# Optimization experiments

Hardware: AMD Instinct MI355X
Metric: run time of the kernel (lower is better)

## Reference

```python
import jax, jax.numpy as jnp
import numpy as np

HIDDEN = 4096
NH = 32        # query heads
HD = 128       # head dim
NKV = 8        # kv heads
RD = 64        # rotary dim (partial rotary)
THETA = 10000.0
SEQ = 2048


def _rope(x, positions):
    # x: [S, H, HD]; neox-style rope on first RD dims of each head
    half = RD // 2
    inv_freq = 1.0 / (THETA ** (jnp.arange(half, dtype=jnp.float32) / half))
    freqs = positions.astype(jnp.float32)[:, None] * inv_freq[None, :]  # [S, half]
    cos = jnp.cos(freqs)[:, None, :]  # [S,1,half]
    sin = jnp.sin(freqs)[:, None, :]
    x_rot, x_pass = x[..., :RD], x[..., RD:]
    x1, x2 = x_rot[..., :half], x_rot[..., half:]
    o1 = x1 * cos - x2 * sin
    o2 = x2 * cos + x1 * sin
    return jnp.concatenate([o1, o2, x_pass], axis=-1)


def setup_inputs() -> dict:
    key = jax.random.key(0)
    k1, k2, k3 = jax.random.split(key, 3)
    hidden_states = jax.random.normal(k1, (SEQ, HIDDEN), dtype=jnp.float32)
    Wqkv = jax.random.normal(k2, (HIDDEN, (NH + 2 * NKV) * HD), dtype=jnp.float32) * 0.02
    Wo = jax.random.normal(k3, (NH * HD, HIDDEN), dtype=jnp.float32) * 0.02
    positions = jnp.arange(SEQ, dtype=jnp.int64)
    return {"hidden_states": hidden_states, "Wqkv": Wqkv, "Wo": Wo, "positions": positions}


def reference(hidden_states, Wqkv, Wo, positions):
    S = hidden_states.shape[0]
    qkv = hidden_states @ Wqkv  # [S, (NH+2*NKV)*HD]
    q, k, v = jnp.split(qkv, [NH * HD, NH * HD + NKV * HD], axis=-1)
    q = q.reshape(S, NH, HD)
    k = k.reshape(S, NKV, HD)
    v = v.reshape(S, NKV, HD)
    q = _rope(q, positions)
    k = _rope(k, positions)
    # GQA: expand kv heads to query heads
    g = NH // NKV
    k = jnp.repeat(k, g, axis=1)  # [S, NH, HD]
    v = jnp.repeat(v, g, axis=1)
    scale = HD ** -0.5
    scores = jnp.einsum('shd,thd->hst', q, k) * scale  # [NH, S, S]
    causal = jnp.tril(jnp.ones((S, S), dtype=bool))
    scores = jnp.where(causal[None, :, :], scores, jnp.finfo(scores.dtype).min)
    probs = jax.nn.softmax(scores, axis=-1)
    attn = jnp.einsum('hst,thd->shd', probs, v).reshape(S, NH * HD)
    return attn @ Wo
```

## Files before the change

kernel.cpp:

```cpp
#include <hip/hip_runtime.h>

#define S_LEN 2048
#define HID 4096
#define NH 32
#define NKV 8
#define HD 128
#define QKVN 6144
#define KOFF 4096
#define VOFF 5120

typedef unsigned short ushort_t;
typedef unsigned int uint_t;
typedef __attribute__((ext_vector_type(8))) short short8;
typedef __attribute__((ext_vector_type(4))) short short4v;
typedef __attribute__((ext_vector_type(4))) float float4_t;

__device__ __forceinline__ float bf2f(ushort_t u) {
    return __uint_as_float(((uint_t)u) << 16);
}
__device__ __forceinline__ uint_t f2bf(float f) {
    uint_t u = __float_as_uint(f);
    u += 0x7fffu + ((u >> 16) & 1u);
    return u >> 16;
}

__device__ __forceinline__ void gload_lds16(const ushort_t* g, ushort_t* l) {
    __builtin_amdgcn_global_load_lds(
        (const __attribute__((address_space(1))) void*)g,
        (__attribute__((address_space(3))) void*)l, 16, 0, 0);
}

__global__ void f32_to_bf16(const float4* __restrict__ in,
                            short4v* __restrict__ out) {
    int i = blockIdx.x * 256 + threadIdx.x;
    float4 v = in[i];
    short4v o;
    o[0] = (short)f2bf(v.x);
    o[1] = (short)f2bf(v.y);
    o[2] = (short)f2bf(v.z);
    o[3] = (short)f2bf(v.w);
    out[i] = o;
}

__global__ void transpose_f32_bf16(const float* __restrict__ in,
                                   ushort_t* __restrict__ out, int R, int C) {
    __shared__ float t[32][33];
    int c0 = blockIdx.x * 32, r0 = blockIdx.y * 32;
    int ci = threadIdx.x & 31, rb = threadIdx.x >> 5;
#pragma unroll
    for (int p = 0; p < 4; p++) {
        int ri = rb + p * 8;
        t[ri][ci] = in[(size_t)(r0 + ri) * C + c0 + ci];
    }
    __syncthreads();
    int cp = (threadIdx.x & 15) * 2;
    int rw = threadIdx.x >> 4;
#pragma unroll
    for (int p = 0; p < 2; p++) {
        int ri = rw + p * 16;
        uint_t w = f2bf(t[cp][ri]) | (f2bf(t[cp + 1][ri]) << 16);
        *(uint_t*)(&out[(size_t)(c0 + ri) * R + r0 + cp]) = w;
    }
}

__global__ __launch_bounds__(256, 2)
void gemm_bf16(const ushort_t* __restrict__ A, const ushort_t* __restrict__ BT,
               float* __restrict__ Cout, int M, int N, int K) {
    __shared__ __attribute__((aligned(16))) ushort_t As[128 * 32];
    __shared__ __attribute__((aligned(16))) ushort_t Bs[128 * 32];
    const int tid  = threadIdx.x;
    const int wave = tid >> 6;
    const int lane = tid & 63;
    const int quad = lane >> 4;
    const int l16  = lane & 15;
    const int m0 = blockIdx.y * 128;
    const int n0 = blockIdx.x * 128;
    const int wm = (wave & 1) * 64;
    const int wn = (wave >> 1) * 64;

    const int r0 = tid >> 2;
    const int kc = (tid & 3) * 8;
    const ushort_t* gA0 = A  + (size_t)(m0 + r0)      * K + kc;
    const ushort_t* gA1 = A  + (size_t)(m0 + r0 + 64) * K + kc;
    const ushort_t* gB0 = BT + (size_t)(n0 + r0)      * K + kc;
    const ushort_t* gB1 = BT + (size_t)(n0 + r0 + 64) * K + kc;
    ushort_t* lA0 = &As[r0 * 32 + kc];
    ushort_t* lA1 = lA0 + 64 * 32;
    ushort_t* lB0 = &Bs[r0 * 32 + kc];
    ushort_t* lB1 = lB0 + 64 * 32;

    float4_t acc[4][4] = {};

    for (int k0 = 0; k0 < K; k0 += 32) {
        gload_lds16(gA0 + k0, lA0);
        gload_lds16(gA1 + k0, lA1);
        gload_lds16(gB0 + k0, lB0);
        gload_lds16(gB1 + k0, lB1);
        __syncthreads();

        short8 af[4], bfr[4];
#pragma unroll
        for (int i = 0; i < 4; i++)
            af[i] = *(const short8*)(&As[(wm + i * 16 + l16) * 32 + quad * 8]);
#pragma unroll
        for (int j = 0; j < 4; j++)
            bfr[j] = *(const short8*)(&Bs[(wn + j * 16 + l16) * 32 + quad * 8]);
#pragma unroll
        for (int i = 0; i < 4; i++)
#pragma unroll
            for (int j = 0; j < 4; j++)
                acc[i][j] = __builtin_amdgcn_mfma_f32_16x16x32_bf16(
                    af[i], bfr[j], acc[i][j], 0, 0, 0);
        __syncthreads();
    }

#pragma unroll
    for (int i = 0; i < 4; i++)
#pragma unroll
        for (int j = 0; j < 4; j++)
#pragma unroll
            for (int r = 0; r < 4; r++) {
                int row = m0 + wm + i * 16 + quad * 4 + r;
                int col = n0 + wn + j * 16 + l16;
                Cout[(size_t)row * N + col] = acc[i][j][r];
            }
}

__global__ void rope_tab_k(float2* __restrict__ tab) {
    int idx = blockIdx.x * 256 + threadIdx.x;
    int i = idx & 31;
    int s = idx >> 5;
    float invf = exp2f(-(float)i * (13.287712379549449f / 32.0f));
    float fr = (float)s * invf;
    float c, sn;
    sincosf(fr, &sn, &c);
    tab[idx] = make_float2(c, sn);
}

#define QSC 0.12753102543918255f
__global__ void prep_q(const float* __restrict__ qkv, const float2* __restrict__ tab,
                       ushort_t* __restrict__ Qb) {
    int idx = blockIdx.x * 256 + threadIdx.x;
    int d = idx & 127;
    int s = (idx >> 7) & 2047;
    int h = idx >> 18;
    const float* row = qkv + (size_t)s * QKVN + h * HD;
    float v;
    if (d < 64) {
        int i = d & 31;
        float2 cs = tab[(s << 5) + i];
        float x1 = row[i], x2 = row[i + 32];
        v = (d < 32) ? (x1 * cs.x - x2 * cs.y) : (x2 * cs.x + x1 * cs.y);
    } else {
        v = row[d];
    }
    Qb[idx] = (ushort_t)f2bf(v * QSC);
}

__global__ void prep_k(const float* __restrict__ qkv, const float2* __restrict__ tab,
                       ushort_t* __restrict__ Kb) {
    int idx = blockIdx.x * 256 + threadIdx.x;
    int d = idx & 127;
    int t = (idx >> 7) & 2047;
    int hk = idx >> 18;
    const float* row = qkv + (size_t)t * QKVN + KOFF + hk * HD;
    float v;
    if (d < 64) {
        int i = d & 31;
        float2 cs = tab[(t << 5) + i];
        float x1 = row[i], x2 = row[i + 32];
        v = (d < 32) ? (x1 * cs.x - x2 * cs.y) : (x2 * cs.x + x1 * cs.y);
    } else {
        v = row[d];
    }
    Kb[idx] = (ushort_t)f2bf(v);
}

__global__ void prep_v(const float* __restrict__ qkv, ushort_t* __restrict__ Vt) {
    __shared__ float tile[32][33];
    int hk = blockIdx.z;
    int t0 = blockIdx.x * 32, d0 = blockIdx.y * 32;
    int ci = threadIdx.x & 31, rb = threadIdx.x >> 5;
#pragma unroll
    for (int p = 0; p < 4; p++) {
        int tr = rb + p * 8;
        tile[tr][ci] = qkv[(size_t)(t0 + tr) * QKVN + VOFF + hk * HD + d0 + ci];
    }
    __syncthreads();
#pragma unroll
    for (int p = 0; p < 4; p++) {
        int dr = rb + p * 8;
        Vt[((size_t)hk * HD + d0 + dr) * S_LEN + t0 + ci] = (ushort_t)f2bf(tile[ci][dr]);
    }
}

__global__ __launch_bounds__(256, 3)
void flash_attn(const ushort_t* __restrict__ Qb, const ushort_t* __restrict__ Kb,
                const ushort_t* __restrict__ Vt, ushort_t* __restrict__ attn) {
    __shared__ __attribute__((aligned(16))) ushort_t Ks[2][32 * 128];
    __shared__ __attribute__((aligned(16))) ushort_t Vs[2][128 * 32];

    const int h    = blockIdx.y;
    const int hk   = h >> 2;
    const int tid  = threadIdx.x;
    const int wave = tid >> 6;
    const int lane = tid & 63;
    const int quad = lane >> 4;
    const int l16  = lane & 15;
    const int bx   = (int)blockIdx.x;
    const int u    = bx + 16 * wave;
    const int qwE  = u * 32;
    const int qwO  = qwE + 16;

    const ushort_t* Qh = Qb + (size_t)h  * S_LEN * HD;
    const ushort_t* Kh = Kb + (size_t)hk * S_LEN * HD;
    const ushort_t* Vh = Vt + (size_t)hk * HD * S_LEN;

    const int krow = tid >> 4;
    const int ksrc = ((tid & 15) ^ (krow & 7)) << 3;
    const ushort_t* gK0 = Kh + (size_t)krow * HD + ksrc;
    const ushort_t* gK1 = Kh + (size_t)(krow + 16) * HD + ksrc;
    const int vrow = tid >> 2;
    const int vtb  = (tid & 3) << 3;
    const ushort_t* gV0 = Vh + (size_t)vrow * S_LEN + vtb;
    const ushort_t* gV1 = Vh + (size_t)(vrow + 64) * S_LEN + vtb;

    ushort_t* lK = &Ks[0][tid * 8];
    ushort_t* lV = &Vs[0][tid * 8];

#define STAGE(buf, t0)                                                        \
    do {                                                                      \
        gload_lds16(gK0 + (size_t)(t0) * HD, lK + (buf) * (32 * 128));        \
        gload_lds16(gK1 + (size_t)(t0) * HD, lK + (buf) * (32 * 128) + 2048); \
        gload_lds16(gV0 + (t0),              lV + (buf) * (128 * 32));        \
        gload_lds16(gV1 + (t0),              lV + (buf) * (128 * 32) + 2048); \
    } while (0)

    short8 qfE[4], qfO[4];
#pragma unroll
    for (int c = 0; c < 4; c++) {
        qfE[c] = *(const short8*)(Qh + (size_t)(qwE + l16) * HD + c * 32 + quad * 8);
        qfO[c] = *(const short8*)(Qh + (size_t)(qwO + l16) * HD + c * 32 + quad * 8);
    }

    float4_t oaccE[8] = {}, oaccO[8] = {};
    float lsumE = 0.f, lsumO = 0.f;
    const int s0 = (((quad * 2)     & 3) << 4) | l16;
    const int s1 = (((quad * 2 + 1) & 3) << 4) | l16;

    const int T0w   = qwE;
    const int T0max = (bx + 48) * 32;
    const int kxor  = (l16 & 7) << 3;

    STAGE(0, 0);
    __syncthreads();

#pragma unroll 1
    for (int t0 = 0; t0 <= T0max; t0 += 32) {
        const int cur = (t0 >> 5) & 1;
        if (t0 + 32 <= T0max) STAGE(cur ^ 1, t0 + 32);

        if (t0 <= T0w) {
            const ushort_t* Kbuf = Ks[cur];
            const ushort_t* Vbuf = Vs[cur];

            float4_t stAE = {}, stBE = {}, stAO = {}, stBO = {};
#pragma unroll
            for (int c = 0; c < 4; c++) {
                short8 kfA = *(const short8*)(Kbuf + l16 * 128 +
                                              ((c * 32 + quad * 8) ^ kxor));
                short8 kfB = *(const short8*)(Kbuf + (16 + l16) * 128 +
                                              ((c * 32 + quad * 8) ^ kxor));
                stAE = __builtin_amdgcn_mfma_f32_16x16x32_bf16(kfA, qfE[c], stAE, 0, 0, 0);
                stAO = __builtin_amdgcn_mfma_f32_16x16x32_bf16(kfA, qfO[c], stAO, 0, 0, 0);
                stBE = __builtin_amdgcn_mfma_f32_16x16x32_bf16(kfB, qfE[c], stBE, 0, 0, 0);
                stBO = __builtin_amdgcn_mfma_f32_16x16x32_bf16(kfB, qfO[c], stBO, 0, 0, 0);
            }

            const bool maskT = (t0 == T0w);
            float pAE[4], pBE[4], pAO[4], pBO[4];
#pragma unroll
            for (int r = 0; r < 4; r++) {
                float eAE = exp2f(stAE[r]);
                float eBE = exp2f(stBE[r]);
                float eAO = exp2f(stAO[r]);
                float eBO = exp2f(stBO[r]);
                if (maskT) {
                    int tA = t0 + quad * 4 + r;
                    eAE = (tA      <= qwE + l16) ? eAE : 0.f;
                    eBE = (tA + 16 <= qwE + l16) ? eBE : 0.f;
                    eAO = (tA      <= qwO + l16) ? eAO : 0.f;
                    eBO = (tA + 16 <= qwO + l16) ? eBO : 0.f;
                }
                pAE[r] = eAE; pBE[r] = eBE;
                pAO[r] = eAO; pBO[r] = eBO;
                lsumE += eAE + eBE;
                lsumO += eAO + eBO;
            }

            short8 pbE, pbO;
            {
                uint_t a01 = f2bf(pAE[0]) | (f2bf(pAE[1]) << 16);
                uint_t a23 = f2bf(pAE[2]) | (f2bf(pAE[3]) << 16);
                uint_t b01 = f2bf(pBE[0]) | (f2bf(pBE[1]) << 16);
                uint_t b23 = f2bf(pBE[2]) | (f2bf(pBE[3]) << 16);
                uint_t A01s0 = (uint_t)__shfl((int)a01, s0);
                uint_t A23s0 = (uint_t)__shfl((int)a23, s0);
                uint_t B01s0 = (uint_t)__shfl((int)b01, s0);
                uint_t B23s0 = (uint_t)__shfl((int)b23, s0);
                uint_t A01s1 = (uint_t)__shfl((int)a01, s1);
                uint_t A23s1 = (uint_t)__shfl((int)a23, s1);
                uint_t B01s1 = (uint_t)__shfl((int)b01, s1);
                uint_t B23s1 = (uint_t)__shfl((int)b23, s1);
                uint_t w[4];
                w[0] = quad < 2 ? A01s0 : B01s0;
                w[1] = quad < 2 ? A23s0 : B23s0;
                w[2] = quad < 2 ? A01s1 : B01s1;
                w[3] = quad < 2 ? A23s1 : B23s1;
                __builtin_memcpy(&pbE, w, 16);
            }
            {
                uint_t a01 = f2bf(pAO[0]) | (f2bf(pAO[1]) << 16);
                uint_t a23 = f2bf(pAO[2]) | (f2bf(pAO[3]) << 16);
                uint_t b01 = f2bf(pBO[0]) | (f2bf(pBO[1]) << 16);
                uint_t b23 = f2bf(pBO[2]) | (f2bf(pBO[3]) << 16);
                uint_t A01s0 = (uint_t)__shfl((int)a01, s0);
                uint_t A23s0 = (uint_t)__shfl((int)a23, s0);
                uint_t B01s0 = (uint_t)__shfl((int)b01, s0);
                uint_t B23s0 = (uint_t)__shfl((int)b23, s0);
                uint_t A01s1 = (uint_t)__shfl((int)a01, s1);
                uint_t A23s1 = (uint_t)__shfl((int)a23, s1);
                uint_t B01s1 = (uint_t)__shfl((int)b01, s1);
                uint_t B23s1 = (uint_t)__shfl((int)b23, s1);
                uint_t w[4];
                w[0] = quad < 2 ? A01s0 : B01s0;
                w[1] = quad < 2 ? A23s0 : B23s0;
                w[2] = quad < 2 ? A01s1 : B01s1;
                w[3] = quad < 2 ? A23s1 : B23s1;
                __builtin_memcpy(&pbO, w, 16);
            }

#pragma unroll
            for (int dt = 0; dt < 8; dt++) {
                short8 vf = *(const short8*)(Vbuf + (dt * 16 + l16) * 32 + quad * 8);
                oaccE[dt] = __builtin_amdgcn_mfma_f32_16x16x32_bf16(vf, pbE, oaccE[dt], 0, 0, 0);
                oaccO[dt] = __builtin_amdgcn_mfma_f32_16x16x32_bf16(vf, pbO, oaccO[dt], 0, 0, 0);
            }
        }

        __syncthreads();
    }
#undef STAGE

    lsumE += __shfl_xor(lsumE, 16);
    lsumE += __shfl_xor(lsumE, 32);
    lsumO += __shfl_xor(lsumO, 16);
    lsumO += __shfl_xor(lsumO, 32);
    float invlE = 1.f / lsumE;
    float invlO = 1.f / lsumO;
    ushort_t* orowE = attn + (size_t)(qwE + l16) * (NH * HD) + h * HD;
    ushort_t* orowO = attn + (size_t)(qwO + l16) * (NH * HD) + h * HD;
#pragma unroll
    for (int dt = 0; dt < 8; dt++) {
        short4v wvE, wvO;
#pragma unroll
        for (int r = 0; r < 4; r++) {
            wvE[r] = (short)f2bf(oaccE[dt][r] * invlE);
            wvO[r] = (short)f2bf(oaccO[dt][r] * invlO);
        }
        *(short4v*)(orowE + dt * 16 + quad * 4) = wvE;
        *(short4v*)(orowO + dt * 16 + quad * 4) = wvO;
    }
}

extern "C" void kernel_launch(void* const* d_in, const int* in_sizes, int n_in,
                              void* d_out, int out_size, void* d_ws, size_t ws_size,
                              hipStream_t stream) {
    const float* hidden = (const float*)d_in[0];
    const float* Wqkv   = (const float*)d_in[1];
    const float* Wo     = (const float*)d_in[2];
    float* out = (float*)d_out;

    char* ws = (char*)d_ws;
    float*    qkv   = (float*)   (ws);
    ushort_t* attnB = (ushort_t*)(ws);
    ushort_t* hidB  = (ushort_t*)(ws + 50331648);
    ushort_t* Qb    = hidB;
    ushort_t* WqkvT = (ushort_t*)(ws + 67108864);
    float2*   rtab  = (float2*)  (ws + 67108864);
    ushort_t* WoT   = (ushort_t*)(ws + 117440512);
    ushort_t* Kb    = (ushort_t*)(ws + 150994944);
    ushort_t* Vt    = (ushort_t*)(ws + 155189248);

    f32_to_bf16<<<(S_LEN * HID) / 1024, 256, 0, stream>>>(
        (const float4*)hidden, (short4v*)hidB);
    transpose_f32_bf16<<<dim3(QKVN / 32, HID / 32), 256, 0, stream>>>(Wqkv, WqkvT, HID, QKVN);
    transpose_f32_bf16<<<dim3(HID / 32, HID / 32), 256, 0, stream>>>(Wo, WoT, HID, HID);

    gemm_bf16<<<dim3(QKVN / 128, S_LEN / 128), 256, 0, stream>>>(
        hidB, WqkvT, qkv, S_LEN, QKVN, HID);

    rope_tab_k<<<(S_LEN * 32) / 256, 256, 0, stream>>>(rtab);
    prep_q<<<(NH  * S_LEN * HD) / 256, 256, 0, stream>>>(qkv, rtab, Qb);
    prep_k<<<(NKV * S_LEN * HD) / 256, 256, 0, stream>>>(qkv, rtab, Kb);
    prep_v<<<dim3(S_LEN / 32, HD / 32, NKV), 256, 0, stream>>>(qkv, Vt);

    flash_attn<<<dim3(16, NH), 256, 0, stream>>>(Qb, Kb, Vt, attnB);

    gemm_bf16<<<dim3(HID / 128, S_LEN / 128), 256, 0, stream>>>(
        attnB, WoT, out, S_LEN, HID, HID);
}
```

Baseline: 569.7 us.

## Fuse RoPE, scaling and bf16 Q/K/V layout writes into QKV GEMM epilogue

The QKV projection GEMM now applies rotary embedding, the Q scale and the bf16 conversion in its epilogue, writing Q and K per head and V transposed directly. This removes the fp32 qkv intermediate (about 50MB written and reread) and three prep kernel launches. The RoPE pair partner is taken from the accumulator tile two 16-column blocks away, which relies on each wave's 64-column span holding exactly one rotary half-pair. The flash_attn launch bound also changes from 3 to 2 waves per EU, which may alter its register allocation and occupancy.

Result: no change. 558.8 us (-1.9%).

```diff
diff --git a/kernel.cpp b/kernel.cpp
--- a/kernel.cpp
+++ b/kernel.cpp
@@ -63,69 +63,6 @@
     }
 }
 
-__global__ __launch_bounds__(256, 2)
-void gemm_bf16(const ushort_t* __restrict__ A, const ushort_t* __restrict__ BT,
-               float* __restrict__ Cout, int M, int N, int K) {
-    __shared__ __attribute__((aligned(16))) ushort_t As[128 * 32];
-    __shared__ __attribute__((aligned(16))) ushort_t Bs[128 * 32];
-    const int tid  = threadIdx.x;
-    const int wave = tid >> 6;
-    const int lane = tid & 63;
-    const int quad = lane >> 4;
-    const int l16  = lane & 15;
-    const int m0 = blockIdx.y * 128;
-    const int n0 = blockIdx.x * 128;
-    const int wm = (wave & 1) * 64;
-    const int wn = (wave >> 1) * 64;
-
-    const int r0 = tid >> 2;
-    const int kc = (tid & 3) * 8;
-    const ushort_t* gA0 = A  + (size_t)(m0 + r0)      * K + kc;
-    const ushort_t* gA1 = A  + (size_t)(m0 + r0 + 64) * K + kc;
-    const ushort_t* gB0 = BT + (size_t)(n0 + r0)      * K + kc;
-    const ushort_t* gB1 = BT + (size_t)(n0 + r0 + 64) * K + kc;
-    ushort_t* lA0 = &As[r0 * 32 + kc];
-    ushort_t* lA1 = lA0 + 64 * 32;
-    ushort_t* lB0 = &Bs[r0 * 32 + kc];
-    ushort_t* lB1 = lB0 + 64 * 32;
-
-    float4_t acc[4][4] = {};
-
-    for (int k0 = 0; k0 < K; k0 += 32) {
-        gload_lds16(gA0 + k0, lA0);
-        gload_lds16(gA1 + k0, lA1);
-        gload_lds16(gB0 + k0, lB0);
-        gload_lds16(gB1 + k0, lB1);
-        __syncthreads();
-
-        short8 af[4], bfr[4];
-#pragma unroll
-        for (int i = 0; i < 4; i++)
-            af[i] = *(const short8*)(&As[(wm + i * 16 + l16) * 32 + quad * 8]);
-#pragma unroll
-        for (int j = 0; j < 4; j++)
-            bfr[j] = *(const short8*)(&Bs[(wn + j * 16 + l16) * 32 + quad * 8]);
-#pragma unroll
-        for (int i = 0; i < 4; i++)
-#pragma unroll
-            for (int j = 0; j < 4; j++)
-                acc[i][j] = __builtin_amdgcn_mfma_f32_16x16x32_bf16(
-                    af[i], bfr[j], acc[i][j], 0, 0, 0);
-        __syncthreads();
-    }
-
-#pragma unroll
-    for (int i = 0; i < 4; i++)
-#pragma unroll
-        for (int j = 0; j < 4; j++)
-#pragma unroll
-            for (int r = 0; r < 4; r++) {
-                int row = m0 + wm + i * 16 + quad * 4 + r;
-                int col = n0 + wn + j * 16 + l16;
-                Cout[(size_t)row * N + col] = acc[i][j][r];
-            }
-}
-
 __global__ void rope_tab_k(float2* __restrict__ tab) {
     int idx = blockIdx.x * 256 + threadIdx.x;
     int i = idx & 31;
@@ -137,64 +74,116 @@
     tab[idx] = make_float2(c, sn);
 }
 
+#define GEMM_BODY(A, BT, K)                                                   \
+    __shared__ __attribute__((aligned(16))) ushort_t As[128 * 32];            \
+    __shared__ __attribute__((aligned(16))) ushort_t Bs[128 * 32];            \
+    const int tid  = threadIdx.x;                                             \
+    const int wave = tid >> 6;                                                \
+    const int lane = tid & 63;                                                \
+    const int quad = lane >> 4;                                               \
+    const int l16  = lane & 15;                                               \
+    const int m0 = blockIdx.y * 128;                                          \
+    const int n0 = blockIdx.x * 128;                                          \
+    const int wm = (wave & 1) * 64;                                           \
+    const int wn = (wave >> 1) * 64;                                          \
+    const int r0 = tid >> 2;                                                  \
+    const int kc = (tid & 3) * 8;                                             \
+    const ushort_t* gA0 = A  + (size_t)(m0 + r0)      * K + kc;               \
+    const ushort_t* gA1 = A  + (size_t)(m0 + r0 + 64) * K + kc;               \
+    const ushort_t* gB0 = BT + (size_t)(n0 + r0)      * K + kc;               \
+    const ushort_t* gB1 = BT + (size_t)(n0 + r0 + 64) * K + kc;               \
+    ushort_t* lA0 = &As[r0 * 32 + kc];                                        \
+    ushort_t* lA1 = lA0 + 64 * 32;                                            \
+    ushort_t* lB0 = &Bs[r0 * 32 + kc];                                        \
+    ushort_t* lB1 = lB0 + 64 * 32;                                            \
+    float4_t acc[4][4] = {};                                                  \
+    for (int k0 = 0; k0 < K; k0 += 32) {                                      \
+        gload_lds16(gA0 + k0, lA0);                                           \
+        gload_lds16(gA1 + k0, lA1);                                           \
+        gload_lds16(gB0 + k0, lB0);                                           \
+        gload_lds16(gB1 + k0, lB1);                                           \
+        __syncthreads();                                                      \
+        short8 af[4], bfr[4];                                                 \
+        _Pragma("unroll")                                                     \
+        for (int i = 0; i < 4; i++)                                           \
+            af[i] = *(const short8*)(&As[(wm + i * 16 + l16) * 32 + quad * 8]);\
+        _Pragma("unroll")                                                     \
+        for (int j = 0; j < 4; j++)                                           \
+            bfr[j] = *(const short8*)(&Bs[(wn + j * 16 + l16) * 32 + quad * 8]);\
+        _Pragma("unroll")                                                     \
+        for (int i = 0; i < 4; i++)                                           \
+            _Pragma("unroll")                                                 \
+            for (int j = 0; j < 4; j++)                                       \
+                acc[i][j] = __builtin_amdgcn_mfma_f32_16x16x32_bf16(          \
+                    af[i], bfr[j], acc[i][j], 0, 0, 0);                       \
+        __syncthreads();                                                      \
+    }
+
+__global__ __launch_bounds__(256, 2)
+void gemm_bf16(const ushort_t* __restrict__ A, const ushort_t* __restrict__ BT,
+               float* __restrict__ Cout, int M, int N, int K) {
+    GEMM_BODY(A, BT, K)
+#pragma unroll
+    for (int i = 0; i < 4; i++)
+#pragma unroll
+        for (int j = 0; j < 4; j++)
+#pragma unroll
+            for (int r = 0; r < 4; r++) {
+                int row = m0 + wm + i * 16 + quad * 4 + r;
+                int col = n0 + wn + j * 16 + l16;
+                Cout[(size_t)row * N + col] = acc[i][j][r];
+            }
+}
+
 #define QSC 0.12753102543918255f
-__global__ void prep_q(const float* __restrict__ qkv, const float2* __restrict__ tab,
-                       ushort_t* __restrict__ Qb) {
-    int idx = blockIdx.x * 256 + threadIdx.x;
-    int d = idx & 127;
-    int s = (idx >> 7) & 2047;
-    int h = idx >> 18;
-    const float* row = qkv + (size_t)s * QKVN + h * HD;
-    float v;
-    if (d < 64) {
-        int i = d & 31;
-        float2 cs = tab[(s << 5) + i];
-        float x1 = row[i], x2 = row[i + 32];
-        v = (d < 32) ? (x1 * cs.x - x2 * cs.y) : (x2 * cs.x + x1 * cs.y);
+__global__ __launch_bounds__(256, 2)
+void gemm_qkv(const ushort_t* __restrict__ A, const ushort_t* __restrict__ BT,
+              const float2* __restrict__ tab, ushort_t* __restrict__ Qb,
+              ushort_t* __restrict__ Kb, ushort_t* __restrict__ Vt) {
+    GEMM_BODY(A, BT, HID)
+    const int ht = n0 >> 7;
+    if (ht < 40) {
+        const bool isQ = (ht < 32);
+        ushort_t* Out = isQ ? (Qb + (size_t)ht * S_LEN * HD)
+                            : (Kb + (size_t)(ht - 32) * S_LEN * HD);
+        const float sc = isQ ? QSC : 1.0f;
+#pragma unroll
+        for (int i = 0; i < 4; i++)
+#pragma unroll
+            for (int j = 0; j < 4; j++) {
+                const int d = wn + j * 16 + l16;
+#pragma unroll
+                for (int r = 0; r < 4; r++) {
+                    const int s = m0 + wm + i * 16 + quad * 4 + r;
+                    float v = acc[i][j][r];
+                    if (d < 64) {
+                        float2 cs = tab[(s << 5) + (d & 31)];
+                        float other = (j < 2) ? acc[i][j + 2][r]
+                                              : acc[i][j - 2][r];
+                        v = (d < 32) ? (v * cs.x - other * cs.y)
+                                     : (v * cs.x + other * cs.y);
+                    }
+                    Out[(size_t)s * HD + d] = (ushort_t)f2bf(v * sc);
+                }
+            }
     } else {
-        v = row[d];
-    }
-    Qb[idx] = (ushort_t)f2bf(v * QSC);
-}
-
-__global__ void prep_k(const float* __restrict__ qkv, const float2* __restrict__ tab,
-                       ushort_t* __restrict__ Kb) {
-    int idx = blockIdx.x * 256 + threadIdx.x;
-    int d = idx & 127;
-    int t = (idx >> 7) & 2047;
-    int hk = idx >> 18;
-    const float* row = qkv + (size_t)t * QKVN + KOFF + hk * HD;
-    float v;
-    if (d < 64) {
-        int i = d & 31;
-        float2 cs = tab[(t << 5) + i];
-        float x1 = row[i], x2 = row[i + 32];
-        v = (d < 32) ? (x1 * cs.x - x2 * cs.y) : (x2 * cs.x + x1 * cs.y);
-    } else {
-        v = row[d];
-    }
-    Kb[idx] = (ushort_t)f2bf(v);
-}
-
-__global__ void prep_v(const float* __restrict__ qkv, ushort_t* __restrict__ Vt) {
-    __shared__ float tile[32][33];
-    int hk = blockIdx.z;
-    int t0 = blockIdx.x * 32, d0 = blockIdx.y * 32;
-    int ci = threadIdx.x & 31, rb = threadIdx.x >> 5;
-#pragma unroll
-    for (int p = 0; p < 4; p++) {
-        int tr = rb + p * 8;
-        tile[tr][ci] = qkv[(size_t)(t0 + tr) * QKVN + VOFF + hk * HD + d0 + ci];
-    }
-    __syncthreads();
-#pragma unroll
-    for (int p = 0; p < 4; p++) {
-        int dr = rb + p * 8;
-        Vt[((size_t)hk * HD + d0 + dr) * S_LEN + t0 + ci] = (ushort_t)f2bf(tile[ci][dr]);
-    }
-}
-
-__global__ __launch_bounds__(256, 3)
+        ushort_t* Vhk = Vt + (size_t)(ht - 40) * HD * S_LEN;
+#pragma unroll
+        for (int i = 0; i < 4; i++)
+#pragma unroll
+            for (int j = 0; j < 4; j++) {
+                const int d  = wn + j * 16 + l16;
+                const int tb = m0 + wm + i * 16 + quad * 4;
+                short4v wv;
+#pragma unroll
+                for (int r = 0; r < 4; r++)
+                    wv[r] = (short)f2bf(acc[i][j][r]);
+                *(short4v*)(Vhk + (size_t)d * S_LEN + tb) = wv;
+            }
+    }
+}
+
+__global__ __launch_bounds__(256, 2)
 void flash_attn(const ushort_t* __restrict__ Qb, const ushort_t* __restrict__ Kb,
                 const ushort_t* __restrict__ Vt, ushort_t* __restrict__ attn) {
     __shared__ __attribute__((aligned(16))) ushort_t Ks[2][32 * 128];
@@ -382,28 +371,23 @@
     float* out = (float*)d_out;
 
     char* ws = (char*)d_ws;
-    float*    qkv   = (float*)   (ws);
     ushort_t* attnB = (ushort_t*)(ws);
+    ushort_t* Qb    = (ushort_t*)(ws + 16777216);
+    ushort_t* Kb    = (ushort_t*)(ws + 33554432);
+    ushort_t* Vt    = (ushort_t*)(ws + 37748736);
+    float2*   rtab  = (float2*)  (ws + 41943040);
     ushort_t* hidB  = (ushort_t*)(ws + 50331648);
-    ushort_t* Qb    = hidB;
     ushort_t* WqkvT = (ushort_t*)(ws + 67108864);
-    float2*   rtab  = (float2*)  (ws + 67108864);
     ushort_t* WoT   = (ushort_t*)(ws + 117440512);
-    ushort_t* Kb    = (ushort_t*)(ws + 150994944);
-    ushort_t* Vt    = (ushort_t*)(ws + 155189248);
 
     f32_to_bf16<<<(S_LEN * HID) / 1024, 256, 0, stream>>>(
         (const float4*)hidden, (short4v*)hidB);
     transpose_f32_bf16<<<dim3(QKVN / 32, HID / 32), 256, 0, stream>>>(Wqkv, WqkvT, HID, QKVN);
     transpose_f32_bf16<<<dim3(HID / 32, HID / 32), 256, 0, stream>>>(Wo, WoT, HID, HID);
-
-    gemm_bf16<<<dim3(QKVN / 128, S_LEN / 128), 256, 0, stream>>>(
-        hidB, WqkvT, qkv, S_LEN, QKVN, HID);
-
     rope_tab_k<<<(S_LEN * 32) / 256, 256, 0, stream>>>(rtab);
-    prep_q<<<(NH  * S_LEN * HD) / 256, 256, 0, stream>>>(qkv, rtab, Qb);
-    prep_k<<<(NKV * S_LEN * HD) / 256, 256, 0, stream>>>(qkv, rtab, Kb);
-    prep_v<<<dim3(S_LEN / 32, HD / 32, NKV), 256, 0, stream>>>(qkv, Vt);
+
+    gemm_qkv<<<dim3(QKVN / 128, S_LEN / 128), 256, 0, stream>>>(
+        hidB, WqkvT, rtab, Qb, Kb, Vt);
 
     flash_attn<<<dim3(16, NH), 256, 0, stream>>>(Qb, Kb, Vt, attnB);
 
```
